# Kernel tuning notes

Hardware: AMD Instinct MI355X
Metric: run time of the kernel (lower is better)

## Reference

```python
import jax, jax.numpy as jnp
import numpy as np

B, T, IN, H = 256, 512, 8, 512  # batch, seq_len, input_size, hidden_size_lstm
MAXV, MINV = 4.2, 2.5


def setup_inputs() -> dict:
    key = jax.random.key(0)
    ks = jax.random.split(key, 14)
    std = 1.0 / np.sqrt(H)
    n = lambda k, sh, s: (jax.random.normal(k, sh, jnp.float32) * s)
    return {
        "u_seq": jax.random.normal(ks[0], (B, T, IN), jnp.float32),
        "w_ih_0": n(ks[1], (4 * H, IN), std),
        "w_hh_0": n(ks[2], (4 * H, H), std),
        "b_ih_0": n(ks[3], (4 * H,), std),
        "b_hh_0": n(ks[4], (4 * H,), std),
        "w_ih_1": n(ks[5], (4 * H, H), std),
        "w_hh_1": n(ks[6], (4 * H, H), std),
        "b_ih_1": n(ks[7], (4 * H,), std),
        "b_hh_1": n(ks[8], (4 * H,), std),
        "fc_w0": n(ks[9], (256, H), std),
        "fc_b0": jnp.zeros((256,), jnp.float32),
        "fc_w1": n(ks[10], (2, 256), std),
        "fc_b1": jnp.zeros((2,), jnp.float32),
    }


def lstm_layer(x, w_ih, w_hh, b_ih, b_hh):
    """x: [B, T, D_in] -> (outputs [B, T, H], last hidden [B, H]).
    PyTorch gate order: input, forget, cell(g), output. h_0 = c_0 = 0."""
    bsz = x.shape[0]
    # Precompute input-to-gate projections for all timesteps: [B, T, 4H]
    xg = jnp.einsum('bti,gi->btg', x, w_ih) + b_ih + b_hh

    def step(carry, xg_t):
        h, c = carry
        gates = xg_t + h @ w_hh.T  # [B, 4H]
        i, f, g, o = jnp.split(gates, 4, axis=-1)
        i = jax.nn.sigmoid(i)
        f = jax.nn.sigmoid(f)
        g = jnp.tanh(g)
        o = jax.nn.sigmoid(o)
        c = f * c + i * g
        h = o * jnp.tanh(c)
        return (h, c), h

    h0 = jnp.zeros((bsz, H), x.dtype)
    (h_T, _), hs = jax.lax.scan(step, (h0, h0), jnp.swapaxes(xg, 0, 1))
    return jnp.swapaxes(hs, 0, 1), h_T


def reference(u_seq, w_ih_0, w_hh_0, b_ih_0, b_hh_0,
              w_ih_1, w_hh_1, b_ih_1, b_hh_1,
              fc_w0, fc_b0, fc_w1, fc_b1):
    out0, _ = lstm_layer(u_seq, w_ih_0, w_hh_0, b_ih_0, b_hh_0)
    _, h_T = lstm_layer(out0, w_ih_1, w_hh_1, b_ih_1, b_hh_1)
    # last_out = out[:, -1, :] == final hidden of top layer
    h = jnp.tanh(h_T @ fc_w0.T + fc_b0)
    x = h @ fc_w1.T + fc_b1
    return (x + 1.0) / 2.0 * (MAXV - MINV) + MINV
```

## Files before the change

### kernel.cpp

```cpp
#include <hip/hip_runtime.h>
#include <stdint.h>

#define HID   512
#define SEQT  512
#define NB    32
#define L1_RB 2064
#define L0_RB 1072
#define BUF1_U64 65536
#define FPAD 16

typedef __attribute__((ext_vector_type(8)))  __bf16 bf16x8;
typedef __attribute__((ext_vector_type(16))) float  f32x16;
typedef unsigned long long u64;

__device__ __forceinline__ unsigned short f2bf(float x) {
  union { float f; unsigned u; } v; v.f = x;
  return (unsigned short)((v.u + 0x7FFFu + ((v.u >> 16) & 1u)) >> 16);
}
__device__ __forceinline__ float bf2f(unsigned short h) {
  union { unsigned u; float f; } v; v.u = ((unsigned)h) << 16;
  return v.f;
}
__device__ __forceinline__ float sigm(float x)     { return 1.0f / (1.0f + __expf(-x)); }
__device__ __forceinline__ float tanhfast(float x) { return 2.0f / (1.0f + __expf(-2.0f * x)) - 1.0f; }

__device__ __forceinline__ u64 ld_agent(const u64* p) {
  return __hip_atomic_load(p, __ATOMIC_RELAXED, __HIP_MEMORY_SCOPE_AGENT);
}
__device__ __forceinline__ void st_agent(u64* p, u64 v) {
  __hip_atomic_store(p, v, __ATOMIC_RELAXED, __HIP_MEMORY_SCOPE_AGENT);
}

__device__ __forceinline__ void dma16(const void* g, void* l) {
  __builtin_amdgcn_global_load_lds((const unsigned int*)g, (unsigned int*)l, 16, 0, 0x11);
}

__global__ __launch_bounds__(256, 1) void lstm_persist(
    const float* __restrict__ u_seq,
    const float* __restrict__ w_ih_0, const float* __restrict__ w_hh_0,
    const float* __restrict__ b_ih_0, const float* __restrict__ b_hh_0,
    const float* __restrict__ w_ih_1, const float* __restrict__ w_hh_1,
    const float* __restrict__ b_ih_1, const float* __restrict__ b_hh_1,
    const float* __restrict__ fc_w0, const float* __restrict__ fc_b0,
    const float* __restrict__ fc_w1, const float* __restrict__ fc_b1,
    float* __restrict__ out, int* flags, u64* hbuf)
{
  extern __shared__ char smemc[];

  const int bid  = blockIdx.x;
  const int g    = bid >> 5;
  const int rr   = bid & 31;
  const int isL1 = rr >> 4;
  const int rl   = rr & 15;
  const int tid  = threadIdx.x;
  const int wv   = tid >> 6;
  const int lane = tid & 63;
  const int lcol = lane & 31;
  const int kh   = lane >> 5;
  const int batch0 = g * NB;

  const int unit_base = rl * 32 + wv * 8;
  const int prow = unit_base * 4 + lcol;
  const int orig = (prow & 3) * HID + (prow >> 2);

  auto groupbar = [&](int gen) {
    __syncthreads();
    if (tid == 0)
      __hip_atomic_store(&flags[bid * FPAD], gen, __ATOMIC_RELAXED, __HIP_MEMORY_SCOPE_AGENT);
    if (tid < 32) {
      const int* fl = flags + (g * 32 + tid) * FPAD;
      while (__hip_atomic_load(fl, __ATOMIC_RELAXED, __HIP_MEMORY_SCOPE_AGENT) < gen)
        __builtin_amdgcn_s_sleep(1);
    }
    __syncthreads();
  };

  {
    u64* p = hbuf + (size_t)bid * 512;
    st_agent(p + tid, 0);
    st_agent(p + tid + 256, 0);
  }
  int gen = 1;
  groupbar(gen++);

  if (isL1) {
    bf16x8 w[64];
    {
      const float* bih = w_ih_1 + (size_t)orig * HID;
      const float* bhh = w_hh_1 + (size_t)orig * HID;
#pragma unroll
      for (int s = 0; s < 64; ++s) {
        int k = s * 16 + kh * 8;
        const float* src = (k < HID) ? (bih + k) : (bhh + (k - HID));
        float4 f0 = *(const float4*)src, f1 = *(const float4*)(src + 4);
        union { bf16x8 v; unsigned short h[8]; } u;
        u.h[0]=f2bf(f0.x); u.h[1]=f2bf(f0.y); u.h[2]=f2bf(f0.z); u.h[3]=f2bf(f0.w);
        u.h[4]=f2bf(f1.x); u.h[5]=f2bf(f1.y); u.h[6]=f2bf(f1.z); u.h[7]=f2bf(f1.w);
        w[s] = u.v;
      }
    }
    float bias[16];
#pragma unroll
    for (int rg = 0; rg < 16; ++rg) {
      int unit = unit_base + 2 * (rg >> 2) + kh;
      int gi = (rg & 3) * HID + unit;
      bias[rg] = b_ih_1[gi] + b_hh_1[gi];
    }
    float cc[4] = {0.f, 0.f, 0.f, 0.f};

    for (int tau = 0; tau <= SEQT; ++tau) {
      const char* curb = (const char*)(hbuf + ((tau & 1) ? BUF1_U64 : 0));
      u64*        nxt  = hbuf + ((tau & 1) ? 0 : BUF1_U64);
      if (tau >= 1) {
#pragma unroll
        for (int j = 0; j < 8; ++j) {
          int b = wv * 8 + j;
          const char* gr = curb + ((size_t)(batch0 + b) << 11) + lane * 16;
          char* lr = smemc + b * L1_RB;
          dma16(gr, lr);
          dma16(gr + 1024, lr + 1024);
        }
        __syncthreads();
        f32x16 a0, a1;
#pragma unroll
        for (int i = 0; i < 16; ++i) { a0[i] = bias[i]; a1[i] = 0.f; }
        const char* brow = smemc + lcol * L1_RB + kh * 16;
#pragma unroll
        for (int s = 0; s < 64; s += 2) {
          bf16x8 b0 = *(const bf16x8*)(brow + s * 32);
          bf16x8 b1 = *(const bf16x8*)(brow + s * 32 + 32);
          a0 = __builtin_amdgcn_mfma_f32_32x32x16_bf16(w[s],     b0, a0, 0, 0, 0);
          a1 = __builtin_amdgcn_mfma_f32_32x32x16_bf16(w[s + 1], b1, a1, 0, 0, 0);
        }
        float hv[4];
#pragma unroll
        for (int q = 0; q < 4; ++q) {
          float ig = sigm(a0[4 * q + 0] + a1[4 * q + 0]);
          float fg = sigm(a0[4 * q + 1] + a1[4 * q + 1]);
          float gg = tanhfast(a0[4 * q + 2] + a1[4 * q + 2]);
          float og = sigm(a0[4 * q + 3] + a1[4 * q + 3]);
          float c = fg * cc[q] + ig * gg;
          cc[q] = c;
          hv[q] = og * tanhfast(c);
        }
        unsigned own01 = (unsigned)f2bf(hv[0]) | ((unsigned)f2bf(hv[1]) << 16);
        unsigned own23 = (unsigned)f2bf(hv[2]) | ((unsigned)f2bf(hv[3]) << 16);
        unsigned p01 = (unsigned)__shfl_xor((int)own01, 32);
        unsigned p23 = (unsigned)__shfl_xor((int)own23, 32);
        if (kh == 0) {
          u64 q0 = ((u64)((own01 & 0xffffu) | ((p01 & 0xffffu) << 16)))
                 | (((u64)((own01 >> 16) | (p01 & 0xffff0000u))) << 32);
          u64 q1 = ((u64)((own23 & 0xffffu) | ((p23 & 0xffffu) << 16)))
                 | (((u64)((own23 >> 16) | (p23 & 0xffff0000u))) << 32);
          u64* orow = nxt + (size_t)(batch0 + lcol) * 256 + 128 + (unit_base >> 2);
          st_agent(orow, q0);
          st_agent(orow + 1, q1);
        }
      }
      groupbar(gen++);
    }
  } else {
    bf16x8 w[33];
    {
      const float* bhh = w_hh_0 + (size_t)orig * HID;
#pragma unroll
      for (int s = 0; s < 32; ++s) {
        int k = s * 16 + kh * 8;
        float4 f0 = *(const float4*)(bhh + k), f1 = *(const float4*)(bhh + k + 4);
        union { bf16x8 v; unsigned short h[8]; } u;
        u.h[0]=f2bf(f0.x); u.h[1]=f2bf(f0.y); u.h[2]=f2bf(f0.z); u.h[3]=f2bf(f0.w);
        u.h[4]=f2bf(f1.x); u.h[5]=f2bf(f1.y); u.h[6]=f2bf(f1.z); u.h[7]=f2bf(f1.w);
        w[s] = u.v;
      }
      {
        union { bf16x8 v; unsigned short h[8]; } u;
        if (kh == 0) {
          const float* src = w_ih_0 + (size_t)orig * 8;
#pragma unroll
          for (int j = 0; j < 8; ++j) u.h[j] = f2bf(src[j]);
        } else {
#pragma unroll
          for (int j = 0; j < 8; ++j) u.h[j] = 0;
        }
        w[32] = u.v;
      }
    }
    float bias[16];
#pragma unroll
    for (int rg = 0; rg < 16; ++rg) {
      int unit = unit_base + 2 * (rg >> 2) + kh;
      int gi = (rg & 3) * HID + unit;
      bias[rg] = b_ih_0[gi] + b_hh_0[gi];
    }
    float cc[4] = {0.f, 0.f, 0.f, 0.f};

    if (tid < 64) *(u64*)(smemc + (tid >> 1) * L0_RB + 1040 + (tid & 1) * 8) = 0;

    for (int tau = 0; tau <= SEQT; ++tau) {
      const char* curb = (const char*)(hbuf + ((tau & 1) ? BUF1_U64 : 0));
      u64*        nxt  = hbuf + ((tau & 1) ? 0 : BUF1_U64);
      if (tau < SEQT) {
#pragma unroll
        for (int j = 0; j < 8; ++j) {
          int b = wv * 8 + j;
          const char* gr = curb + ((size_t)(batch0 + b) << 11) + lane * 16;
          dma16(gr, smemc + b * L0_RB);
        }
        {
          int b = tid >> 3, i = tid & 7;
          ((unsigned short*)(smemc + b * L0_RB))[512 + i] =
              f2bf(u_seq[((size_t)(batch0 + b) * SEQT + tau) * 8 + i]);
        }
        __syncthreads();
        f32x16 a0, a1;
#pragma unroll
        for (int i = 0; i < 16; ++i) { a0[i] = bias[i]; a1[i] = 0.f; }
        const char* brow = smemc + lcol * L0_RB + kh * 16;
#pragma unroll
        for (int s = 0; s < 32; s += 2) {
          bf16x8 b0 = *(const bf16x8*)(brow + s * 32);
          bf16x8 b1 = *(const bf16x8*)(brow + s * 32 + 32);
          a0 = __builtin_amdgcn_mfma_f32_32x32x16_bf16(w[s],     b0, a0, 0, 0, 0);
          a1 = __builtin_amdgcn_mfma_f32_32x32x16_bf16(w[s + 1], b1, a1, 0, 0, 0);
        }
        {
          bf16x8 b2 = *(const bf16x8*)(brow + 32 * 32);
          a0 = __builtin_amdgcn_mfma_f32_32x32x16_bf16(w[32], b2, a0, 0, 0, 0);
        }
        float hv[4];
#pragma unroll
        for (int q = 0; q < 4; ++q) {
          float ig = sigm(a0[4 * q + 0] + a1[4 * q + 0]);
          float fg = sigm(a0[4 * q + 1] + a1[4 * q + 1]);
          float gg = tanhfast(a0[4 * q + 2] + a1[4 * q + 2]);
          float og = sigm(a0[4 * q + 3] + a1[4 * q + 3]);
          float c = fg * cc[q] + ig * gg;
          cc[q] = c;
          hv[q] = og * tanhfast(c);
        }
        unsigned own01 = (unsigned)f2bf(hv[0]) | ((unsigned)f2bf(hv[1]) << 16);
        unsigned own23 = (unsigned)f2bf(hv[2]) | ((unsigned)f2bf(hv[3]) << 16);
        unsigned p01 = (unsigned)__shfl_xor((int)own01, 32);
        unsigned p23 = (unsigned)__shfl_xor((int)own23, 32);
        if (kh == 0) {
          u64 q0 = ((u64)((own01 & 0xffffu) | ((p01 & 0xffffu) << 16)))
                 | (((u64)((own01 >> 16) | (p01 & 0xffff0000u))) << 32);
          u64 q1 = ((u64)((own23 & 0xffffu) | ((p23 & 0xffffu) << 16)))
                 | (((u64)((own23 >> 16) | (p23 & 0xffff0000u))) << 32);
          u64* orow = nxt + (size_t)(batch0 + lcol) * 256 + (unit_base >> 2);
          st_agent(orow, q0);
          st_agent(orow + 1, q1);
        }
      }
      groupbar(gen++);
    }
  }

  {
    float* hT  = (float*)smemc;
    float* hfc = ((float*)smemc) + 512;
    const u64* hrow = hbuf + BUF1_U64 + (size_t)bid * 256 + 128;
    if (tid < 128) {
      u64 v = ld_agent(hrow + tid);
      const unsigned short* s4 = (const unsigned short*)&v;
      hT[tid * 4 + 0] = bf2f(s4[0]);
      hT[tid * 4 + 1] = bf2f(s4[1]);
      hT[tid * 4 + 2] = bf2f(s4[2]);
      hT[tid * 4 + 3] = bf2f(s4[3]);
    }
    __syncthreads();
    {
      float s = fc_b0[tid];
      const float4* wrow = (const float4*)(fc_w0 + (size_t)tid * HID);
#pragma unroll 4
      for (int k4 = 0; k4 < 128; ++k4) {
        float4 wq = wrow[k4];
        s += hT[4 * k4 + 0] * wq.x + hT[4 * k4 + 1] * wq.y +
             hT[4 * k4 + 2] * wq.z + hT[4 * k4 + 3] * wq.w;
      }
      hfc[tid] = tanhfast(s);
    }
    __syncthreads();
    if (tid < 64) {
#pragma unroll
      for (int kk = 0; kk < 2; ++kk) {
        float p = 0.f;
        for (int j = tid; j < 256; j += 64) p += hfc[j] * fc_w1[kk * 256 + j];
#pragma unroll
        for (int off = 32; off; off >>= 1) p += __shfl_down(p, off, 64);
        if (tid == 0) out[bid * 2 + kk] = p * 0.85f + (fc_b1[kk] * 0.85f + 3.35f);
      }
    }
  }
}

extern "C" void kernel_launch(void* const* d_in, const int* in_sizes, int n_in,
                              void* d_out, int out_size, void* d_ws, size_t ws_size,
                              hipStream_t stream) {
  const float* u_seq  = (const float*)d_in[0];
  const float* w_ih_0 = (const float*)d_in[1];
  const float* w_hh_0 = (const float*)d_in[2];
  const float* b_ih_0 = (const float*)d_in[3];
  const float* b_hh_0 = (const float*)d_in[4];
  const float* w_ih_1 = (const float*)d_in[5];
  const float* w_hh_1 = (const float*)d_in[6];
  const float* b_ih_1 = (const float*)d_in[7];
  const float* b_hh_1 = (const float*)d_in[8];
  const float* fc_w0  = (const float*)d_in[9];
  const float* fc_b0  = (const float*)d_in[10];
  const float* fc_w1  = (const float*)d_in[11];
  const float* fc_b1  = (const float*)d_in[12];
  float* out = (float*)d_out;

  int* flags = (int*)d_ws;
  u64* hbuf  = (u64*)((char*)d_ws + 16384);

  size_t shmem = (size_t)NB * L1_RB;
  hipFuncSetAttribute((const void*)lstm_persist,
                      hipFuncAttributeMaxDynamicSharedMemorySize, (int)shmem);
  hipLaunchKernelGGL(lstm_persist, dim3(256), dim3(256), shmem, stream,
                     u_seq, w_ih_0, w_hh_0, b_ih_0, b_hh_0,
                     w_ih_1, w_hh_1, b_ih_1, b_hh_1,
                     fc_w0, fc_b0, fc_w1, fc_b1, out, flags, hbuf);
}
```

Before: 2.517 ms.

## Replace group-wide barrier with per-wave generation flags and double-buffered LDS

Drops the per-timestep group barrier, in which every block stored a flag and then spun until all 32 blocks in its group had arrived. Instead, each wave publishes a monotonically increasing generation counter per buffer once its stores have drained, and consumers spin on only the counters for the buffer they read. LDS staging is double-buffered by timestep parity, so a block can start the next step without a trailing __syncthreads. This cuts barrier latency and lets the layer-0 and layer-1 blocks run further out of step, at the cost of relying on relaxed atomics plus waitcnt for memory ordering, which is fragile, and of doubling the shared memory footprint.

```diff
diff --git a/kernel.cpp b/kernel.cpp
--- a/kernel.cpp
+++ b/kernel.cpp
@@ -6,8 +6,9 @@
 #define NB    32
 #define L1_RB 2064
 #define L0_RB 1072
+#define L1_HALF (NB * L1_RB)
+#define L0_HALF (NB * L0_RB)
 #define BUF1_U64 65536
-#define FPAD 16
 
 typedef __attribute__((ext_vector_type(8)))  __bf16 bf16x8;
 typedef __attribute__((ext_vector_type(16))) float  f32x16;
@@ -43,7 +44,7 @@
     const float* __restrict__ b_ih_1, const float* __restrict__ b_hh_1,
     const float* __restrict__ fc_w0, const float* __restrict__ fc_b0,
     const float* __restrict__ fc_w1, const float* __restrict__ fc_b1,
-    float* __restrict__ out, int* flags, u64* hbuf)
+    float* __restrict__ out, u64* arr, u64* hbuf)
 {
   extern __shared__ char smemc[];
 
@@ -63,25 +64,23 @@
   const int prow = unit_base * 4 + lcol;
   const int orig = (prow & 3) * HID + (prow >> 2);
 
-  auto groupbar = [&](int gen) {
-    __syncthreads();
-    if (tid == 0)
-      __hip_atomic_store(&flags[bid * FPAD], gen, __ATOMIC_RELAXED, __HIP_MEMORY_SCOPE_AGENT);
-    if (tid < 32) {
-      const int* fl = flags + (g * 32 + tid) * FPAD;
-      while (__hip_atomic_load(fl, __ATOMIC_RELAXED, __HIP_MEMORY_SCOPE_AGENT) < gen)
-        __builtin_amdgcn_s_sleep(1);
-    }
-    __syncthreads();
+  auto poll = [&](int bufidx, int gen) {
+    const long long* a = (const long long*)(arr + (size_t)((g * 2 + bufidx) * 128));
+    const long long ge = gen;
+    for (;;) {
+      long long v0 = __hip_atomic_load(a + lane,      __ATOMIC_RELAXED, __HIP_MEMORY_SCOPE_AGENT);
+      long long v1 = __hip_atomic_load(a + 64 + lane, __ATOMIC_RELAXED, __HIP_MEMORY_SCOPE_AGENT);
+      if (__all((v0 >= ge) && (v1 >= ge))) break;
+    }
+    asm volatile("" ::: "memory");
   };
 
-  {
-    u64* p = hbuf + (size_t)bid * 512;
-    st_agent(p + tid, 0);
-    st_agent(p + tid + 256, 0);
-  }
-  int gen = 1;
-  groupbar(gen++);
+  auto signal = [&](int bufidx, int tile, int val) {
+    asm volatile("s_waitcnt vmcnt(0) lgkmcnt(0)" ::: "memory");
+    if (lane == 0)
+      __hip_atomic_store((long long*)(arr + (size_t)((g * 2 + bufidx) * 128 + tile * 4 + wv)),
+                         (long long)val, __ATOMIC_RELAXED, __HIP_MEMORY_SCOPE_AGENT);
+  };
 
   if (isL1) {
     bf16x8 w[64];
@@ -106,58 +105,71 @@
       int gi = (rg & 3) * HID + unit;
       bias[rg] = b_ih_1[gi] + b_hh_1[gi];
     }
+
+    {
+      u64* nxt = hbuf + BUF1_U64;
+      if (kh == 0) {
+        u64* orow = nxt + (size_t)(batch0 + lcol) * 256 + 128 + (unit_base >> 2);
+        st_agent(orow, 0);
+        st_agent(orow + 1, 0);
+      }
+      signal(1, 16 + rl, 1);
+    }
+
     float cc[4] = {0.f, 0.f, 0.f, 0.f};
 
-    for (int tau = 0; tau <= SEQT; ++tau) {
+    for (int tau = 1; tau <= SEQT; ++tau) {
       const char* curb = (const char*)(hbuf + ((tau & 1) ? BUF1_U64 : 0));
       u64*        nxt  = hbuf + ((tau & 1) ? 0 : BUF1_U64);
-      if (tau >= 1) {
-#pragma unroll
-        for (int j = 0; j < 8; ++j) {
-          int b = wv * 8 + j;
-          const char* gr = curb + ((size_t)(batch0 + b) << 11) + lane * 16;
-          char* lr = smemc + b * L1_RB;
-          dma16(gr, lr);
-          dma16(gr + 1024, lr + 1024);
-        }
-        __syncthreads();
-        f32x16 a0, a1;
-#pragma unroll
-        for (int i = 0; i < 16; ++i) { a0[i] = bias[i]; a1[i] = 0.f; }
-        const char* brow = smemc + lcol * L1_RB + kh * 16;
-#pragma unroll
-        for (int s = 0; s < 64; s += 2) {
-          bf16x8 b0 = *(const bf16x8*)(brow + s * 32);
-          bf16x8 b1 = *(const bf16x8*)(brow + s * 32 + 32);
-          a0 = __builtin_amdgcn_mfma_f32_32x32x16_bf16(w[s],     b0, a0, 0, 0, 0);
-          a1 = __builtin_amdgcn_mfma_f32_32x32x16_bf16(w[s + 1], b1, a1, 0, 0, 0);
-        }
-        float hv[4];
-#pragma unroll
-        for (int q = 0; q < 4; ++q) {
-          float ig = sigm(a0[4 * q + 0] + a1[4 * q + 0]);
-          float fg = sigm(a0[4 * q + 1] + a1[4 * q + 1]);
-          float gg = tanhfast(a0[4 * q + 2] + a1[4 * q + 2]);
-          float og = sigm(a0[4 * q + 3] + a1[4 * q + 3]);
-          float c = fg * cc[q] + ig * gg;
-          cc[q] = c;
-          hv[q] = og * tanhfast(c);
-        }
-        unsigned own01 = (unsigned)f2bf(hv[0]) | ((unsigned)f2bf(hv[1]) << 16);
-        unsigned own23 = (unsigned)f2bf(hv[2]) | ((unsigned)f2bf(hv[3]) << 16);
-        unsigned p01 = (unsigned)__shfl_xor((int)own01, 32);
-        unsigned p23 = (unsigned)__shfl_xor((int)own23, 32);
-        if (kh == 0) {
-          u64 q0 = ((u64)((own01 & 0xffffu) | ((p01 & 0xffffu) << 16)))
-                 | (((u64)((own01 >> 16) | (p01 & 0xffff0000u))) << 32);
-          u64 q1 = ((u64)((own23 & 0xffffu) | ((p23 & 0xffffu) << 16)))
-                 | (((u64)((own23 >> 16) | (p23 & 0xffff0000u))) << 32);
-          u64* orow = nxt + (size_t)(batch0 + lcol) * 256 + 128 + (unit_base >> 2);
-          st_agent(orow, q0);
-          st_agent(orow + 1, q1);
-        }
-      }
-      groupbar(gen++);
+      char*       half = smemc + (tau & 1) * L1_HALF;
+
+      poll(tau & 1, tau);
+#pragma unroll
+      for (int j = 0; j < 8; ++j) {
+        int b = wv * 8 + j;
+        const char* gr = curb + ((size_t)(batch0 + b) << 11) + lane * 16;
+        char* lr = half + b * L1_RB;
+        dma16(gr, lr);
+        dma16(gr + 1024, lr + 1024);
+      }
+      __syncthreads();
+
+      f32x16 a0, a1;
+#pragma unroll
+      for (int i = 0; i < 16; ++i) { a0[i] = bias[i]; a1[i] = 0.f; }
+      const char* brow = half + lcol * L1_RB + kh * 16;
+#pragma unroll
+      for (int s = 0; s < 64; s += 2) {
+        bf16x8 b0 = *(const bf16x8*)(brow + s * 32);
+        bf16x8 b1 = *(const bf16x8*)(brow + s * 32 + 32);
+        a0 = __builtin_amdgcn_mfma_f32_32x32x16_bf16(w[s],     b0, a0, 0, 0, 0);
+        a1 = __builtin_amdgcn_mfma_f32_32x32x16_bf16(w[s + 1], b1, a1, 0, 0, 0);
+      }
+      float hv[4];
+#pragma unroll
+      for (int q = 0; q < 4; ++q) {
+        float ig = sigm(a0[4 * q + 0] + a1[4 * q + 0]);
+        float fg = sigm(a0[4 * q + 1] + a1[4 * q + 1]);
+        float gg = tanhfast(a0[4 * q + 2] + a1[4 * q + 2]);
+        float og = sigm(a0[4 * q + 3] + a1[4 * q + 3]);
+        float c = fg * cc[q] + ig * gg;
+        cc[q] = c;
+        hv[q] = og * tanhfast(c);
+      }
+      unsigned own01 = (unsigned)f2bf(hv[0]) | ((unsigned)f2bf(hv[1]) << 16);
+      unsigned own23 = (unsigned)f2bf(hv[2]) | ((unsigned)f2bf(hv[3]) << 16);
+      unsigned p01 = (unsigned)__shfl_xor((int)own01, 32);
+      unsigned p23 = (unsigned)__shfl_xor((int)own23, 32);
+      if (kh == 0) {
+        u64 q0 = ((u64)((own01 & 0xffffu) | ((p01 & 0xffffu) << 16)))
+               | (((u64)((own01 >> 16) | (p01 & 0xffff0000u))) << 32);
+        u64 q1 = ((u64)((own23 & 0xffffu) | ((p23 & 0xffffu) << 16)))
+               | (((u64)((own23 >> 16) | (p23 & 0xffff0000u))) << 32);
+        u64* orow = nxt + (size_t)(batch0 + lcol) * 256 + 128 + (unit_base >> 2);
+        st_agent(orow, q0);
+        st_agent(orow + 1, q1);
+      }
+      signal((tau + 1) & 1, 16 + rl, tau + 1);
     }
   } else {
     bf16x8 w[33];
@@ -194,68 +206,90 @@
     }
     float cc[4] = {0.f, 0.f, 0.f, 0.f};
 
-    if (tid < 64) *(u64*)(smemc + (tid >> 1) * L0_RB + 1040 + (tid & 1) * 8) = 0;
-
-    for (int tau = 0; tau <= SEQT; ++tau) {
+    if (tid < 128) {
+      int h = tid >> 6, t2 = tid & 63;
+      *(u64*)(smemc + h * L0_HALF + (t2 >> 1) * L0_RB + 1040 + (t2 & 1) * 8) = 0;
+    }
+    {
+      u64* r = (u64*)(smemc + (tid >> 3) * L0_RB);
+      int o = (tid & 7) * 16;
+#pragma unroll
+      for (int jj = 0; jj < 16; ++jj) r[o + jj] = 0;
+    }
+
+    for (int tau = 0; tau < SEQT; ++tau) {
       const char* curb = (const char*)(hbuf + ((tau & 1) ? BUF1_U64 : 0));
       u64*        nxt  = hbuf + ((tau & 1) ? 0 : BUF1_U64);
-      if (tau < SEQT) {
+      char*       half = smemc + (tau & 1) * L0_HALF;
+
+      if (tau >= 1) {
+        poll(tau & 1, tau);
 #pragma unroll
         for (int j = 0; j < 8; ++j) {
           int b = wv * 8 + j;
           const char* gr = curb + ((size_t)(batch0 + b) << 11) + lane * 16;
-          dma16(gr, smemc + b * L0_RB);
+          dma16(gr, half + b * L0_RB);
         }
-        {
-          int b = tid >> 3, i = tid & 7;
-          ((unsigned short*)(smemc + b * L0_RB))[512 + i] =
-              f2bf(u_seq[((size_t)(batch0 + b) * SEQT + tau) * 8 + i]);
-        }
-        __syncthreads();
-        f32x16 a0, a1;
-#pragma unroll
-        for (int i = 0; i < 16; ++i) { a0[i] = bias[i]; a1[i] = 0.f; }
-        const char* brow = smemc + lcol * L0_RB + kh * 16;
-#pragma unroll
-        for (int s = 0; s < 32; s += 2) {
-          bf16x8 b0 = *(const bf16x8*)(brow + s * 32);
-          bf16x8 b1 = *(const bf16x8*)(brow + s * 32 + 32);
-          a0 = __builtin_amdgcn_mfma_f32_32x32x16_bf16(w[s],     b0, a0, 0, 0, 0);
-          a1 = __builtin_amdgcn_mfma_f32_32x32x16_bf16(w[s + 1], b1, a1, 0, 0, 0);
-        }
-        {
-          bf16x8 b2 = *(const bf16x8*)(brow + 32 * 32);
-          a0 = __builtin_amdgcn_mfma_f32_32x32x16_bf16(w[32], b2, a0, 0, 0, 0);
-        }
-        float hv[4];
-#pragma unroll
-        for (int q = 0; q < 4; ++q) {
-          float ig = sigm(a0[4 * q + 0] + a1[4 * q + 0]);
-          float fg = sigm(a0[4 * q + 1] + a1[4 * q + 1]);
-          float gg = tanhfast(a0[4 * q + 2] + a1[4 * q + 2]);
-          float og = sigm(a0[4 * q + 3] + a1[4 * q + 3]);
-          float c = fg * cc[q] + ig * gg;
-          cc[q] = c;
-          hv[q] = og * tanhfast(c);
-        }
-        unsigned own01 = (unsigned)f2bf(hv[0]) | ((unsigned)f2bf(hv[1]) << 16);
-        unsigned own23 = (unsigned)f2bf(hv[2]) | ((unsigned)f2bf(hv[3]) << 16);
-        unsigned p01 = (unsigned)__shfl_xor((int)own01, 32);
-        unsigned p23 = (unsigned)__shfl_xor((int)own23, 32);
-        if (kh == 0) {
-          u64 q0 = ((u64)((own01 & 0xffffu) | ((p01 & 0xffffu) << 16)))
-                 | (((u64)((own01 >> 16) | (p01 & 0xffff0000u))) << 32);
-          u64 q1 = ((u64)((own23 & 0xffffu) | ((p23 & 0xffffu) << 16)))
-                 | (((u64)((own23 >> 16) | (p23 & 0xffff0000u))) << 32);
-          u64* orow = nxt + (size_t)(batch0 + lcol) * 256 + (unit_base >> 2);
-          st_agent(orow, q0);
-          st_agent(orow + 1, q1);
-        }
-      }
-      groupbar(gen++);
+      }
+      {
+        int b = tid >> 3, i = tid & 7;
+        ((unsigned short*)(half + b * L0_RB))[512 + i] =
+            f2bf(u_seq[((size_t)(batch0 + b) * SEQT + tau) * 8 + i]);
+      }
+      __syncthreads();
+
+      f32x16 a0, a1;
+#pragma unroll
+      for (int i = 0; i < 16; ++i) { a0[i] = bias[i]; a1[i] = 0.f; }
+      const char* brow = half + lcol * L0_RB + kh * 16;
+#pragma unroll
+      for (int s = 0; s < 32; s += 2) {
+        bf16x8 b0 = *(const bf16x8*)(brow + s * 32);
+        bf16x8 b1 = *(const bf16x8*)(brow + s * 32 + 32);
+        a0 = __builtin_amdgcn_mfma_f32_32x32x16_bf16(w[s],     b0, a0, 0, 0, 0);
+        a1 = __builtin_amdgcn_mfma_f32_32x32x16_bf16(w[s + 1], b1, a1, 0, 0, 0);
+      }
+      {
+        bf16x8 b2 = *(const bf16x8*)(brow + 32 * 32);
+        a0 = __builtin_amdgcn_mfma_f32_32x32x16_bf16(w[32], b2, a0, 0, 0, 0);
+      }
+      float hv[4];
+#pragma unroll
+      for (int q = 0; q < 4; ++q) {
+        float ig = sigm(a0[4 * q + 0] + a1[4 * q + 0]);
+        float fg = sigm(a0[4 * q + 1] + a1[4 * q + 1]);
+        float gg = tanhfast(a0[4 * q + 2] + a1[4 * q + 2]);
+        float og = sigm(a0[4 * q + 3] + a1[4 * q + 3]);
+        float c = fg * cc[q] + ig * gg;
+        cc[q] = c;
+        hv[q] = og * tanhfast(c);
+      }
+      unsigned own01 = (unsigned)f2bf(hv[0]) | ((unsigned)f2bf(hv[1]) << 16);
+      unsigned own23 = (unsigned)f2bf(hv[2]) | ((unsigned)f2bf(hv[3]) << 16);
+      unsigned p01 = (unsigned)__shfl_xor((int)own01, 32);
+      unsigned p23 = (unsigned)__shfl_xor((int)own23, 32);
+      if (kh == 0) {
+        u64 q0 = ((u64)((own01 & 0xffffu) | ((p01 & 0xffffu) << 16)))
+               | (((u64)((own01 >> 16) | (p01 & 0xffff0000u))) << 32);
+        u64 q1 = ((u64)((own23 & 0xffffu) | ((p23 & 0xffffu) << 16)))
+               | (((u64)((own23 >> 16) | (p23 & 0xffff0000u))) << 32);
+        u64* orow = nxt + (size_t)(batch0 + lcol) * 256 + (unit_base >> 2);
+        st_agent(orow, q0);
+        st_agent(orow + 1, q1);
+      }
+      signal((tau + 1) & 1, rl, tau + 1);
     }
   }
 
+  __syncthreads();
+  {
+    const long long* a = (const long long*)(arr + (size_t)((g * 2 + 1) * 128));
+    for (;;) {
+      long long v = __hip_atomic_load(a + 64 + lane, __ATOMIC_RELAXED, __HIP_MEMORY_SCOPE_AGENT);
+      if (__all(v >= SEQT + 1)) break;
+    }
+    asm volatile("" ::: "memory");
+  }
   {
     float* hT  = (float*)smemc;
     float* hfc = ((float*)smemc) + 512;
@@ -312,14 +346,14 @@
   const float* fc_b1  = (const float*)d_in[12];
   float* out = (float*)d_out;
 
-  int* flags = (int*)d_ws;
-  u64* hbuf  = (u64*)((char*)d_ws + 16384);
-
-  size_t shmem = (size_t)NB * L1_RB;
+  u64* arr  = (u64*)d_ws;
+  u64* hbuf = (u64*)((char*)d_ws + 16384);
+
+  size_t shmem = 2 * (size_t)L1_HALF;
   hipFuncSetAttribute((const void*)lstm_persist,
                       hipFuncAttributeMaxDynamicSharedMemorySize, (int)shmem);
   hipLaunchKernelGGL(lstm_persist, dim3(256), dim3(256), shmem, stream,
                      u_seq, w_ih_0, w_hh_0, b_ih_0, b_hh_0,
                      w_ih_1, w_hh_1, b_ih_1, b_hh_1,
-                     fc_w0, fc_b0, fc_w1, fc_b1, out, flags, hbuf);
-}
+                     fc_w0, fc_b0, fc_w1, fc_b1, out, arr, hbuf);
+}
```

After: 4.313 ms. +71.4%, slower.
